# Optimization experiments

Measured on AMD Instinct MI355X. Metric: run time of the kernel, lower is better.

Reference implementation:

```python
import jax, jax.numpy as jnp
import numpy as np

N_NODES = 100000
N_EDGES = 3200000
N_GRAPHS = 2048
VOCAB = 92
H = 64
N_LAYERS = 3


def setup_inputs() -> dict:
    key = jax.random.key(0)
    ks = jax.random.split(key, 16)
    x = jax.random.randint(ks[0], (N_NODES,), 0, VOCAB)
    edge_index = jax.random.randint(ks[1], (2, N_EDGES), 0, N_NODES)
    batch = jnp.sort(jax.random.randint(ks[2], (N_NODES,), 0, N_GRAPHS))
    s = 0.1
    return {
        "x": x,
        "edge_index": edge_index,
        "batch": batch,
        "emb": jax.random.normal(ks[3], (VOCAB, H), jnp.float32) * s,
        "conv_w": jax.random.normal(ks[4], (N_LAYERS, H, H), jnp.float32) * s,
        "conv_b": jax.random.normal(ks[5], (N_LAYERS, H), jnp.float32) * s,
        "w1": jax.random.normal(ks[6], (H, H // 2), jnp.float32) * s,
        "b1": jax.random.normal(ks[7], (H // 2,), jnp.float32) * s,
        "w2": jax.random.normal(ks[8], (H // 2, H // 4), jnp.float32) * s,
        "b2": jax.random.normal(ks[9], (H // 4,), jnp.float32) * s,
        "w3": jax.random.normal(ks[10], (H // 4, 1), jnp.float32) * s,
        "b3": jax.random.normal(ks[11], (1,), jnp.float32) * s,
    }


def _gcn_graph(edge_index, n_nodes):
    # add self-loops, then symmetric degree normalization (PyG GCNConv default)
    loop = jnp.arange(n_nodes)
    row = jnp.concatenate([edge_index[0], loop])  # source
    col = jnp.concatenate([edge_index[1], loop])  # target (aggregation index)
    deg = jnp.zeros((n_nodes,), jnp.float32).at[col].add(1.0)
    dinv = jnp.where(deg > 0, jax.lax.rsqrt(deg), 0.0)
    norm = dinv[row] * dinv[col]  # [E+N]
    return row, col, norm


def _forward(x, edge_index, batch, emb, conv_w, conv_b, w1, b1, w2, b2, w3, b3):
    n = x.shape[0]
    row, col, norm = _gcn_graph(edge_index, n)
    h = emb[x]  # [N,H] embedding lookup
    for i in range(N_LAYERS):
        t = h @ conv_w[i]  # linear transform first (GCNConv)
        msg = t[row] * norm[:, None]  # gather + edge scaling
        agg = jax.ops.segment_sum(msg, col, num_segments=n)  # scatter-add
        h_new = jax.nn.relu(agg + conv_b[i])
        h = h_new if i == 0 else h + h_new  # residual after first layer
    # global mean pool over graphs
    sums = jax.ops.segment_sum(h, batch, num_segments=N_GRAPHS)
    cnt = jax.ops.segment_sum(jnp.ones((n,), h.dtype), batch, num_segments=N_GRAPHS)
    g = sums / jnp.maximum(cnt, 1.0)[:, None]  # [G,H]
    # predictor MLP (dropout is identity in eval)
    g = jax.nn.relu(g @ w1 + b1)
    g = jax.nn.relu(g @ w2 + b2)
    return g @ w3 + b3  # [G,1]


def reference(x, edge_index, batch, emb, conv_w, conv_b, w1, b1, w2, b2, w3, b3):
    return _forward(x, edge_index, batch, emb, conv_w, conv_b, w1, b1, w2, b2, w3, b3)
```

## Files before the change

### kernel.cpp

```cpp
#include <hip/hip_runtime.h>

#define N_NODES 100000
#define N_EDGES 3200000
#define N_GRAPHS 2048
#define VOCAB 92
#define H 64
#define N_LAYERS 3

#define BUCK_BITS 7
#define BUCK_NODES (1 << BUCK_BITS)
#define NBUCK ((N_NODES + BUCK_NODES - 1) / BUCK_NODES)

#define PART_BLOCKS 256
#define EDGES_PER_PART (N_EDGES / PART_BLOCKS)

#define G0_TILE 64
#define SBINS_STRIDE 100
#define SB_STRIDE 104

#define FL_TILE 64
#define A_STRIDE 72

typedef _Float16 half8 __attribute__((ext_vector_type(8)));
typedef float f32x4 __attribute__((ext_vector_type(4)));

__device__ inline unsigned short f2bf(float f) {
    union { float f; unsigned u; } v; v.f = f;
    unsigned u = v.u;
    u += 0x7fffu + ((u >> 16) & 1u);
    return (unsigned short)(u >> 16);
}
__device__ inline float bfhi(unsigned p) {
    union { unsigned u; float f; } v; v.u = p & 0xffff0000u; return v.f;
}
__device__ inline float bflo(unsigned p) {
    union { unsigned u; float f; } v; v.u = p << 16; return v.f;
}

__device__ inline void unpack_add(uint4 v, float* a) {
    a[0] += bflo(v.x); a[1] += bfhi(v.x);
    a[2] += bflo(v.y); a[3] += bfhi(v.y);
    a[4] += bflo(v.z); a[5] += bfhi(v.z);
    a[6] += bflo(v.w); a[7] += bfhi(v.w);
}


__global__ void k_init(int* bcnt, int* srpad) {
    int i = threadIdx.x;
    if (i < NBUCK) bcnt[i] = 0;
    if (i < 16) srpad[i] = 0;
}

__global__ void k_bhist(const int* __restrict__ col, int* __restrict__ bcnt,
                        int* __restrict__ blkhist) {
    __shared__ int lh[NBUCK];
    int tid = threadIdx.x;
    for (int i = tid; i < NBUCK; i += 256) lh[i] = 0;
    __syncthreads();
    int base = blockIdx.x * EDGES_PER_PART;
    for (int k = tid; k < EDGES_PER_PART; k += 256)
        atomicAdd(&lh[col[base + k] >> BUCK_BITS], 1);
    __syncthreads();
    int* myhist = blkhist + (size_t)blockIdx.x * NBUCK;
    for (int i = tid; i < NBUCK; i += 256) {
        int c = lh[i];
        myhist[i] = c;
        if (c) atomicAdd(&bcnt[i], c);
    }
}

__global__ void k_bscan(const int* __restrict__ bcnt, int* __restrict__ bbase,
                        int* __restrict__ bcur) {
    __shared__ int s[1024];
    int tid = threadIdx.x;
    int v = (tid < NBUCK) ? bcnt[tid] : 0;
    s[tid] = v;
    __syncthreads();
    for (int off = 1; off < 1024; off <<= 1) {
        int x = (tid >= off) ? s[tid - off] : 0;
        __syncthreads();
        s[tid] += x;
        __syncthreads();
    }
    if (tid < NBUCK) {
        int e = s[tid] - v;
        bbase[tid] = e;
        bcur[tid] = e;
    }
    if (tid == 0) bbase[NBUCK] = N_EDGES;
}

__global__ __launch_bounds__(1024) void k_binA(const int* __restrict__ row,
                                               const int* __restrict__ col,
                                               const int* __restrict__ blkhist,
                                               int* __restrict__ bcur,
                                               int* __restrict__ staging) {
    __shared__ int lcnt[NBUCK];
    __shared__ int lbase[NBUCK];
    int tid = threadIdx.x;
    int base = blockIdx.x * EDGES_PER_PART;
    const int* myhist = blkhist + (size_t)blockIdx.x * NBUCK;
    for (int i = tid; i < NBUCK; i += 1024) {
        int c = myhist[i];
        lbase[i] = c ? atomicAdd(&bcur[i], c) : 0;
        lcnt[i] = 0;
    }
    __syncthreads();
    for (int k = tid; k < EDGES_PER_PART; k += 1024) {
        int c = col[base + k];
        int b = c >> BUCK_BITS;
        int r = atomicAdd(&lcnt[b], 1);
        staging[lbase[b] + r] = row[base + k] | ((c & (BUCK_NODES - 1)) << 17);
    }
}

__global__ void k_binB(const int* __restrict__ staging, const int* __restrict__ bbase,
                       const int* __restrict__ x,
                       int* __restrict__ sorted_row, int* __restrict__ degi,
                       int* __restrict__ row_start, float* __restrict__ dinv,
                       unsigned* __restrict__ packed) {
    __shared__ int lde[BUCK_NODES];
    __shared__ int lsc[BUCK_NODES];
    int b = blockIdx.x, tid = threadIdx.x;
    int n0 = b << BUCK_BITS;
    int s0 = bbase[b], s1 = bbase[b + 1];
    if (tid < BUCK_NODES) lde[tid] = 0;
    __syncthreads();
    for (int i = s0 + tid; i < s1; i += 256)
        atomicAdd(&lde[staging[i] >> 17], 1);
    __syncthreads();
    if (tid < BUCK_NODES) lsc[tid] = lde[tid];
    __syncthreads();
    for (int off = 1; off < BUCK_NODES; off <<= 1) {
        int v = (tid >= off && tid < BUCK_NODES) ? lsc[tid - off] : 0;
        __syncthreads();
        if (tid < BUCK_NODES) lsc[tid] += v;
        __syncthreads();
    }
    if (tid < BUCK_NODES) {
        int n = n0 + tid;
        int excl = lsc[tid] - lde[tid];
        if (n < N_NODES) {
            row_start[n] = s0 + excl;
            degi[n] = lde[tid];
            float dv = rsqrtf((float)(lde[tid] + 1));
            dinv[n] = dv;
            packed[n] = ((unsigned)f2bf(dv) << 16) | (unsigned)x[n];
        }
        lsc[tid] = excl;
        lde[tid] = 0;
    }
    __syncthreads();
    for (int i = s0 + tid; i < s1; i += 256) {
        int p = staging[i];
        int ln = p >> 17;
        int r = atomicAdd(&lde[ln], 1);
        sorted_row[s0 + lsc[ln] + r] = p & 0x1FFFF;
    }
}

__global__ void k_premix(const float* __restrict__ emb, const float* __restrict__ W0,
                         float* __restrict__ M) {
    int v = blockIdx.x, c = threadIdx.x;
    float acc = 0.0f;
#pragma unroll
    for (int k = 0; k < H; ++k) acc += emb[v * H + k] * W0[k * H + c];
    M[v * H + c] = acc;
}

__global__ __launch_bounds__(256) void k_gather0_mfma(
    const int* __restrict__ sorted_row, const int* __restrict__ row_start,
    const int* __restrict__ degi, const unsigned* __restrict__ packed,
    const float* __restrict__ M, const float* __restrict__ dinv,
    const float* __restrict__ bias, float* __restrict__ h,
    unsigned short* __restrict__ qout) {
    __shared__ float Sbins[G0_TILE][SBINS_STRIDE];
    __shared__ _Float16 Sb[G0_TILE][SB_STRIDE];
    __shared__ _Float16 Blds[H][SB_STRIDE];
    __shared__ int sstart[G0_TILE];
    __shared__ int sdeg[G0_TILE];

    int tid = threadIdx.x;
    int n0 = blockIdx.x * G0_TILE;

    for (int i = tid; i < G0_TILE * SBINS_STRIDE; i += 256)
        ((float*)Sbins)[i] = 0.0f;
    {
        int c = tid & 63, v0 = tid >> 6;
        for (int v = v0; v < VOCAB; v += 4)
            Blds[c][v] = (_Float16)M[v * H + c];
        Blds[c][VOCAB + v0] = (_Float16)0.0f;
    }
    if (tid < G0_TILE) {
        int n = n0 + tid;
        sdeg[tid] = (n < N_NODES) ? degi[n] : 0;
        sstart[tid] = (n < N_NODES) ? row_start[n] : 0;
    }
    __syncthreads();

    int w = tid >> 6, lane = tid & 63;

    if (tid < G0_TILE) {
        int n = n0 + tid;
        if (n < N_NODES) {
            unsigned p = packed[n];
            atomicAdd(&Sbins[tid][p & 127u], __uint_as_float(p & 0xffff0000u));
        }
    }
    for (int ni = 0; ni < 16; ++ni) {
        int nl = (w << 4) + ni;
        int d = sdeg[nl];
        int st = sstart[nl];
        for (int e = lane; e < d; e += 64) {
            unsigned p = packed[sorted_row[st + e]];
            atomicAdd(&Sbins[nl][p & 127u], __uint_as_float(p & 0xffff0000u));
        }
    }
    __syncthreads();

    {
        int r0 = tid >> 2, k0 = (tid & 3) * 24;
#pragma unroll
        for (int m = 0; m < 3; ++m) {
            f32x4 f0 = *(const f32x4*)&Sbins[r0][k0 + 8 * m];
            f32x4 f1 = *(const f32x4*)&Sbins[r0][k0 + 8 * m + 4];
            half8 o;
            o[0] = (_Float16)f0[0]; o[1] = (_Float16)f0[1];
            o[2] = (_Float16)f0[2]; o[3] = (_Float16)f0[3];
            o[4] = (_Float16)f1[0]; o[5] = (_Float16)f1[1];
            o[6] = (_Float16)f1[2]; o[7] = (_Float16)f1[3];
            *(half8*)&Sb[r0][k0 + 8 * m] = o;
        }
    }
    __syncthreads();

    int l15 = lane & 15, l4 = lane >> 4;
    half8 afr[3];
#pragma unroll
    for (int ks = 0; ks < 3; ++ks)
        afr[ks] = *(const half8*)&Sb[(w << 4) + l15][ks * 32 + l4 * 8];

    f32x4 acc[4];
#pragma unroll
    for (int c = 0; c < 4; ++c) {
        f32x4 a = {0.0f, 0.0f, 0.0f, 0.0f};
#pragma unroll
        for (int ks = 0; ks < 3; ++ks) {
            half8 bfr = *(const half8*)&Blds[c * 16 + l15][ks * 32 + l4 * 8];
            a = __builtin_amdgcn_mfma_f32_16x16x32_f16(afr[ks], bfr, a, 0, 0, 0);
        }
        acc[c] = a;
    }

    int rbase = (w << 4) + l4 * 4;
    float di4[4];
#pragma unroll
    for (int r = 0; r < 4; ++r) {
        int n = n0 + rbase + r;
        di4[r] = (n < N_NODES) ? dinv[n] : 0.0f;
    }
#pragma unroll
    for (int c = 0; c < 4; ++c) {
        float bb = bias[c * 16 + l15];
#pragma unroll
        for (int r = 0; r < 4; ++r) {
            int n = n0 + rbase + r;
            if (n < N_NODES) {
                float v = fmaxf(acc[c][r] * di4[r] + bb, 0.0f);
                h[(size_t)n * H + c * 16 + l15] = v;
                qout[(size_t)n * H + c * 16 + l15] = f2bf(di4[r] * v);
            }
        }
    }
}

__global__ __launch_bounds__(256) void k_fused(
    const int* __restrict__ sorted_row, const int* __restrict__ row_start,
    const int* __restrict__ degi, const unsigned* __restrict__ q,
    const float* __restrict__ dinv, const float* __restrict__ W,
    const float* __restrict__ bias, float* __restrict__ h,
    unsigned short* __restrict__ qout, int last) {
    __shared__ _Float16 Alds[FL_TILE][A_STRIDE];
    __shared__ _Float16 Blds[H][A_STRIDE];

    int tid = threadIdx.x;
    int n0 = blockIdx.x * FL_TILE;

    {
        int c = tid & 63, k0 = (tid >> 6) * 16;
#pragma unroll
        for (int k = 0; k < 16; ++k)
            Blds[c][k0 + k] = (_Float16)W[(k0 + k) * H + c];
    }

    int w = tid >> 6, lane = tid & 63;
    int s = lane >> 3;
    int j = lane & 7;
    const uint4* q4 = (const uint4*)q;

    for (int ni = 0; ni < 16; ++ni) {
        int nl = (w << 4) + ni;
        int n = n0 + nl;
        int d = 0, st = 0;
        if (n < N_NODES) { d = degi[n]; st = row_start[n]; }
        const int* srp = sorted_row + st;
        float a[8];
#pragma unroll
        for (int k = 0; k < 8; ++k) a[k] = 0.0f;

        int e = 0;
        for (; e + 16 <= d; e += 16) {
            int srA = srp[e + s];
            int srB = srp[e + 8 + s];
            uint4 va = q4[(size_t)srA * 8 + j];
            uint4 vb = q4[(size_t)srB * 8 + j];
            unpack_add(va, a);
            unpack_add(vb, a);
        }
        if (e < d) {
            int eA = e + s, eB = e + 8 + s;
            int srA = srp[eA];
            int srB = srp[eB];
            uint4 va = q4[(size_t)srA * 8 + j];
            uint4 vb = q4[(size_t)srB * 8 + j];
            if (eA >= d) { va.x = 0; va.y = 0; va.z = 0; va.w = 0; }
            if (eB >= d) { vb.x = 0; vb.y = 0; vb.z = 0; vb.w = 0; }
            unpack_add(va, a);
            unpack_add(vb, a);
        }
#pragma unroll
        for (int k = 0; k < 8; ++k) a[k] += __shfl_xor(a[k], 8, 64);
#pragma unroll
        for (int k = 0; k < 8; ++k) a[k] += __shfl_xor(a[k], 16, 64);
#pragma unroll
        for (int k = 0; k < 8; ++k) a[k] += __shfl_xor(a[k], 32, 64);
        if (s == 0) {
            if (n < N_NODES) {
                uint4 vs = q4[(size_t)n * 8 + j];
                unpack_add(vs, a);
            }
            half8 o;
#pragma unroll
            for (int k = 0; k < 8; ++k) o[k] = (_Float16)a[k];
            *(half8*)&Alds[nl][j * 8] = o;
        }
    }
    __syncthreads();

    int l15 = lane & 15, l4 = lane >> 4;
    half8 afr[2];
#pragma unroll
    for (int ks = 0; ks < 2; ++ks)
        afr[ks] = *(const half8*)&Alds[(w << 4) + l15][ks * 32 + l4 * 8];

    f32x4 acc[4];
#pragma unroll
    for (int c = 0; c < 4; ++c) {
        f32x4 a = {0.0f, 0.0f, 0.0f, 0.0f};
#pragma unroll
        for (int ks = 0; ks < 2; ++ks) {
            half8 bfr = *(const half8*)&Blds[c * 16 + l15][ks * 32 + l4 * 8];
            a = __builtin_amdgcn_mfma_f32_16x16x32_f16(afr[ks], bfr, a, 0, 0, 0);
        }
        acc[c] = a;
    }

    int rbase = (w << 4) + l4 * 4;
    float di4[4];
#pragma unroll
    for (int r = 0; r < 4; ++r) {
        int n = n0 + rbase + r;
        di4[r] = (n < N_NODES) ? dinv[n] : 0.0f;
    }
#pragma unroll
    for (int c = 0; c < 4; ++c) {
        float bb = bias[c * 16 + l15];
#pragma unroll
        for (int r = 0; r < 4; ++r) {
            int n = n0 + rbase + r;
            if (n < N_NODES) {
                size_t idx = (size_t)n * H + c * 16 + l15;
                float v = h[idx] + fmaxf(acc[c][r] * di4[r] + bb, 0.0f);
                h[idx] = v;
                if (!last) qout[idx] = f2bf(di4[r] * v);
            }
        }
    }
}

__global__ void k_poolmlp(const float* __restrict__ h, const int* __restrict__ batch,
                          const float* __restrict__ w1, const float* __restrict__ b1,
                          const float* __restrict__ w2, const float* __restrict__ b2,
                          const float* __restrict__ w3, const float* __restrict__ b3,
                          float* __restrict__ out) {
    __shared__ float sg[H];
    __shared__ float s1[32];
    __shared__ float s2[16];
    int g = blockIdx.x, tid = threadIdx.x;
    int lo = 0, hi = N_NODES;
    while (lo < hi) { int mid = (lo + hi) >> 1; if (batch[mid] < g) lo = mid + 1; else hi = mid; }
    int lo2 = lo, hi2 = N_NODES;
    while (lo2 < hi2) { int mid = (lo2 + hi2) >> 1; if (batch[mid] < g + 1) lo2 = mid + 1; else hi2 = mid; }
    float acc = 0.0f;
    for (int n = lo; n < lo2; ++n) acc += h[(size_t)n * H + tid];
    float cntf = (float)(lo2 - lo);
    sg[tid] = acc / fmaxf(cntf, 1.0f);
    __syncthreads();
    if (tid < 32) {
        float a = b1[tid];
#pragma unroll
        for (int k = 0; k < H; ++k) a += sg[k] * w1[k * 32 + tid];
        s1[tid] = fmaxf(a, 0.0f);
    }
    __syncthreads();
    if (tid < 16) {
        float a = b2[tid];
#pragma unroll
        for (int k = 0; k < 32; ++k) a += s1[k] * w2[k * 16 + tid];
        s2[tid] = fmaxf(a, 0.0f);
    }
    __syncthreads();
    if (tid == 0) {
        float a = b3[0];
#pragma unroll
        for (int k = 0; k < 16; ++k) a += s2[k] * w3[k];
        out[g] = a;
    }
}


extern "C" void kernel_launch(void* const* d_in, const int* in_sizes, int n_in,
                              void* d_out, int out_size, void* d_ws, size_t ws_size,
                              hipStream_t stream) {
    const int*   x      = (const int*)d_in[0];
    const int*   eidx   = (const int*)d_in[1];
    const int*   batch  = (const int*)d_in[2];
    const float* emb    = (const float*)d_in[3];
    const float* conv_w = (const float*)d_in[4];
    const float* conv_b = (const float*)d_in[5];
    const float* w1     = (const float*)d_in[6];
    const float* b1     = (const float*)d_in[7];
    const float* w2     = (const float*)d_in[8];
    const float* b2     = (const float*)d_in[9];
    const float* w3     = (const float*)d_in[10];
    const float* b3     = (const float*)d_in[11];
    float* out = (float*)d_out;

    const int* row = eidx;
    const int* col = eidx + N_EDGES;

    char* wsb = (char*)d_ws;
    size_t off = 0;
    auto alloc = [&](size_t elems) { void* p = wsb + off; off += ((elems * 4 + 255) & ~(size_t)255); return p; };
    int*      bcnt       = (int*)alloc(NBUCK);
    int*      bbase      = (int*)alloc(NBUCK + 1);
    int*      bcur       = (int*)alloc(NBUCK);
    int*      blkhist    = (int*)alloc((size_t)PART_BLOCKS * NBUCK);
    int*      row_start  = (int*)alloc(N_NODES);
    int*      degi       = (int*)alloc(N_NODES);
    float*    dinv       = (float*)alloc(N_NODES);
    unsigned* packed     = (unsigned*)alloc(N_NODES);
    float*    M          = (float*)alloc(VOCAB * H);
    int*      sorted_row = (int*)alloc(N_EDGES + 16);
    float*    h          = (float*)alloc((size_t)N_NODES * H);
    unsigned short* qa   = (unsigned short*)alloc((size_t)N_NODES * H / 2);
    unsigned short* qb   = (unsigned short*)alloc((size_t)N_NODES * H / 2);

    int* staging = (int*)qa;

    const int B = 256;
    const int gT = (N_NODES + FL_TILE - 1) / FL_TILE;

    hipLaunchKernelGGL(k_init, dim3(1), dim3(1024), 0, stream, bcnt, sorted_row + N_EDGES);
    hipLaunchKernelGGL(k_bhist, dim3(PART_BLOCKS), dim3(256), 0, stream, col, bcnt, blkhist);
    hipLaunchKernelGGL(k_bscan, dim3(1), dim3(1024), 0, stream, bcnt, bbase, bcur);
    hipLaunchKernelGGL(k_binA, dim3(PART_BLOCKS), dim3(1024), 0, stream,
                       row, col, blkhist, bcur, staging);
    hipLaunchKernelGGL(k_binB, dim3(NBUCK), dim3(256), 0, stream, staging, bbase, x,
                       sorted_row, degi, row_start, dinv, packed);

    hipLaunchKernelGGL(k_premix, dim3(VOCAB), dim3(H), 0, stream, emb, conv_w, M);
    hipLaunchKernelGGL(k_gather0_mfma, dim3(gT), dim3(B), 0, stream,
                       sorted_row, row_start, degi, packed, M, dinv, conv_b, h, qa);

    hipLaunchKernelGGL(k_fused, dim3(gT), dim3(B), 0, stream,
                       sorted_row, row_start, degi, (const unsigned*)qa, dinv,
                       conv_w + (size_t)1 * H * H, conv_b + 1 * H, h, qb, 0);
    hipLaunchKernelGGL(k_fused, dim3(gT), dim3(B), 0, stream,
                       sorted_row, row_start, degi, (const unsigned*)qb, dinv,
                       conv_w + (size_t)2 * H * H, conv_b + 2 * H, h, qa, 1);

    hipLaunchKernelGGL(k_poolmlp, dim3(N_GRAPHS), dim3(64), 0, stream,
                       h, batch, w1, b1, w2, b2, w3, b3, out);

    (void)in_sizes; (void)n_in; (void)out_size; (void)ws_size;
}
```

Measured before the change: 381.1 us.

## Halve fused-layer tile, prefetch edge indices, use nontemporal loads and stores

The fused gather+MFMA layer kernel now handles 32 nodes per block instead of 64, with 8 nodes per wave, and sets launch_bounds for higher occupancy. Only two waves run the MFMA epilogue. The sorted_row indices for the next 16 edges are software-prefetched with nontemporal loads while the current q gathers are in flight. The h read-modify-write and the q output use nontemporal access so they do not pollute cache. The grid for the first-layer kernel is decoupled from the fused tile. The costs are that half the waves idle in the epilogue, the B-matrix staging runs twice as often, and the prefetch reads past the end of short neighbour lists, which relies on the padding after sorted_row.

```diff
diff --git a/kernel.cpp b/kernel.cpp
--- a/kernel.cpp
+++ b/kernel.cpp
@@ -18,7 +18,7 @@
 #define SBINS_STRIDE 100
 #define SB_STRIDE 104
 
-#define FL_TILE 64
+#define FL_TILE 32
 #define A_STRIDE 72
 
 typedef _Float16 half8 __attribute__((ext_vector_type(8)));
@@ -274,7 +274,7 @@
     }
 }
 
-__global__ __launch_bounds__(256) void k_fused(
+__global__ __launch_bounds__(256, 8) void k_fused(
     const int* __restrict__ sorted_row, const int* __restrict__ row_start,
     const int* __restrict__ degi, const unsigned* __restrict__ q,
     const float* __restrict__ dinv, const float* __restrict__ W,
@@ -298,8 +298,8 @@
     int j = lane & 7;
     const uint4* q4 = (const uint4*)q;
 
-    for (int ni = 0; ni < 16; ++ni) {
-        int nl = (w << 4) + ni;
+    for (int ni = 0; ni < 8; ++ni) {
+        int nl = (w << 3) + ni;
         int n = n0 + nl;
         int d = 0, st = 0;
         if (n < N_NODES) { d = degi[n]; st = row_start[n]; }
@@ -308,23 +308,22 @@
 #pragma unroll
         for (int k = 0; k < 8; ++k) a[k] = 0.0f;
 
+        int srA = __builtin_nontemporal_load(&srp[s]);
+        int srB = __builtin_nontemporal_load(&srp[8 + s]);
         int e = 0;
         for (; e + 16 <= d; e += 16) {
-            int srA = srp[e + s];
-            int srB = srp[e + 8 + s];
             uint4 va = q4[(size_t)srA * 8 + j];
             uint4 vb = q4[(size_t)srB * 8 + j];
+            srA = __builtin_nontemporal_load(&srp[e + 16 + s]);
+            srB = __builtin_nontemporal_load(&srp[e + 24 + s]);
             unpack_add(va, a);
             unpack_add(vb, a);
         }
         if (e < d) {
-            int eA = e + s, eB = e + 8 + s;
-            int srA = srp[eA];
-            int srB = srp[eB];
             uint4 va = q4[(size_t)srA * 8 + j];
             uint4 vb = q4[(size_t)srB * 8 + j];
-            if (eA >= d) { va.x = 0; va.y = 0; va.z = 0; va.w = 0; }
-            if (eB >= d) { vb.x = 0; vb.y = 0; vb.z = 0; vb.w = 0; }
+            if (e + s >= d) { va.x = 0; va.y = 0; va.z = 0; va.w = 0; }
+            if (e + 8 + s >= d) { vb.x = 0; vb.y = 0; vb.z = 0; vb.w = 0; }
             unpack_add(va, a);
             unpack_add(vb, a);
         }
@@ -347,42 +346,46 @@
     }
     __syncthreads();
 
-    int l15 = lane & 15, l4 = lane >> 4;
-    half8 afr[2];
-#pragma unroll
-    for (int ks = 0; ks < 2; ++ks)
-        afr[ks] = *(const half8*)&Alds[(w << 4) + l15][ks * 32 + l4 * 8];
-
-    f32x4 acc[4];
-#pragma unroll
-    for (int c = 0; c < 4; ++c) {
-        f32x4 a = {0.0f, 0.0f, 0.0f, 0.0f};
-#pragma unroll
-        for (int ks = 0; ks < 2; ++ks) {
-            half8 bfr = *(const half8*)&Blds[c * 16 + l15][ks * 32 + l4 * 8];
-            a = __builtin_amdgcn_mfma_f32_16x16x32_f16(afr[ks], bfr, a, 0, 0, 0);
-        }
-        acc[c] = a;
-    }
-
-    int rbase = (w << 4) + l4 * 4;
-    float di4[4];
-#pragma unroll
-    for (int r = 0; r < 4; ++r) {
-        int n = n0 + rbase + r;
-        di4[r] = (n < N_NODES) ? dinv[n] : 0.0f;
-    }
-#pragma unroll
-    for (int c = 0; c < 4; ++c) {
-        float bb = bias[c * 16 + l15];
+    if (w < 2) {
+        int l15 = lane & 15, l4 = lane >> 4;
+        half8 afr[2];
+#pragma unroll
+        for (int ks = 0; ks < 2; ++ks)
+            afr[ks] = *(const half8*)&Alds[(w << 4) + l15][ks * 32 + l4 * 8];
+
+        f32x4 acc[4];
+#pragma unroll
+        for (int c = 0; c < 4; ++c) {
+            f32x4 a = {0.0f, 0.0f, 0.0f, 0.0f};
+#pragma unroll
+            for (int ks = 0; ks < 2; ++ks) {
+                half8 bfr = *(const half8*)&Blds[c * 16 + l15][ks * 32 + l4 * 8];
+                a = __builtin_amdgcn_mfma_f32_16x16x32_f16(afr[ks], bfr, a, 0, 0, 0);
+            }
+            acc[c] = a;
+        }
+
+        int rbase = (w << 4) + l4 * 4;
+        float di4[4];
 #pragma unroll
         for (int r = 0; r < 4; ++r) {
             int n = n0 + rbase + r;
-            if (n < N_NODES) {
-                size_t idx = (size_t)n * H + c * 16 + l15;
-                float v = h[idx] + fmaxf(acc[c][r] * di4[r] + bb, 0.0f);
-                h[idx] = v;
-                if (!last) qout[idx] = f2bf(di4[r] * v);
+            di4[r] = (n < N_NODES) ? dinv[n] : 0.0f;
+        }
+#pragma unroll
+        for (int c = 0; c < 4; ++c) {
+            float bb = bias[c * 16 + l15];
+#pragma unroll
+            for (int r = 0; r < 4; ++r) {
+                int n = n0 + rbase + r;
+                if (n < N_NODES) {
+                    size_t idx = (size_t)n * H + c * 16 + l15;
+                    float v = __builtin_nontemporal_load(&h[idx]) +
+                              fmaxf(acc[c][r] * di4[r] + bb, 0.0f);
+                    __builtin_nontemporal_store(v, &h[idx]);
+                    if (!last)
+                        __builtin_nontemporal_store(f2bf(di4[r] * v), &qout[idx]);
+                }
             }
         }
     }
@@ -469,7 +472,8 @@
     int* staging = (int*)qa;
 
     const int B = 256;
-    const int gT = (N_NODES + FL_TILE - 1) / FL_TILE;
+    const int gT = (N_NODES + G0_TILE - 1) / G0_TILE;
+    const int gF = (N_NODES + FL_TILE - 1) / FL_TILE;
 
     hipLaunchKernelGGL(k_init, dim3(1), dim3(1024), 0, stream, bcnt, sorted_row + N_EDGES);
     hipLaunchKernelGGL(k_bhist, dim3(PART_BLOCKS), dim3(256), 0, stream, col, bcnt, blkhist);
@@ -483,10 +487,10 @@
     hipLaunchKernelGGL(k_gather0_mfma, dim3(gT), dim3(B), 0, stream,
                        sorted_row, row_start, degi, packed, M, dinv, conv_b, h, qa);
 
-    hipLaunchKernelGGL(k_fused, dim3(gT), dim3(B), 0, stream,
+    hipLaunchKernelGGL(k_fused, dim3(gF), dim3(B), 0, stream,
                        sorted_row, row_start, degi, (const unsigned*)qa, dinv,
                        conv_w + (size_t)1 * H * H, conv_b + 1 * H, h, qb, 0);
-    hipLaunchKernelGGL(k_fused, dim3(gT), dim3(B), 0, stream,
+    hipLaunchKernelGGL(k_fused, dim3(gF), dim3(B), 0, stream,
                        sorted_row, row_start, degi, (const unsigned*)qb, dinv,
                        conv_w + (size_t)2 * H * H, conv_b + 2 * H, h, qa, 1);
 
```

New measurement: 415.6 us. +9.0%, slower.
